# Kernel optimization log

Measured on AMD Instinct MI355X. Metric: run time of the kernel, lower is better.

## Reference

```python
import jax, jax.numpy as jnp
import numpy as np

KH = KW = 3  # kernel size for both convs


def conv2d_valid(x, w, b):
    # x: [B,C,H,W], w: [O,C,KH,KW], VALID padding, stride 1 (matches nn.Conv2d(3,18,3))
    y = jax.lax.conv_general_dilated(x, w, window_strides=(1, 1), padding='VALID',
                                     dimension_numbers=('NCHW', 'OIHW', 'NCHW'))
    return y + b[None, :, None, None]


def deform_conv2d(x, offset, w, b):
    # Faithful torchvision deform_conv2d: stride 1, pad 0, dilation 1, 1 group, 1 offset group.
    B, C, H, W = x.shape
    O = w.shape[0]
    Ho, Wo = offset.shape[2], offset.shape[3]
    K = KH * KW
    # offset layout: [B, 2*K, Ho, Wo], per-tap (dy, dx) interleaved, taps row-major
    off = offset.reshape(B, K, 2, Ho, Wo)
    dy, dx = off[:, :, 0], off[:, :, 1]                      # [B,K,Ho,Wo]
    ky = jnp.repeat(jnp.arange(KH), KW).astype(x.dtype)       # [K] tap row
    kx = jnp.tile(jnp.arange(KW), KH).astype(x.dtype)         # [K] tap col
    py = dy + jnp.arange(Ho, dtype=x.dtype)[None, None, :, None] + ky[None, :, None, None]
    px = dx + jnp.arange(Wo, dtype=x.dtype)[None, None, None, :] + kx[None, :, None, None]

    y0 = jnp.floor(py); x0 = jnp.floor(px)
    wy = py - y0; wx = px - x0                                # bilinear fractions
    y0i = y0.astype(jnp.int32); x0i = x0.astype(jnp.int32)

    x_flat = x.reshape(B, C, H * W)

    def corner(yi, xi):
        valid = ((yi >= 0) & (yi < H) & (xi >= 0) & (xi < W)).astype(x.dtype)  # zero pad outside
        idx = jnp.clip(yi, 0, H - 1) * W + jnp.clip(xi, 0, W - 1)              # [B,K,Ho,Wo]
        g = jax.vmap(lambda xf, ix: xf[:, ix])(x_flat, idx)                    # [B,C,K,Ho,Wo]
        return g * valid[:, None]

    val = (corner(y0i, x0i)         * ((1 - wy) * (1 - wx))[:, None]
         + corner(y0i, x0i + 1)     * ((1 - wy) * wx)[:, None]
         + corner(y0i + 1, x0i)     * (wy * (1 - wx))[:, None]
         + corner(y0i + 1, x0i + 1) * (wy * wx)[:, None])     # [B,C,K,Ho,Wo]

    out = jnp.einsum('bckhw,ock->bohw', val, w.reshape(O, C, K))
    return out + b[None, :, None, None]


def setup_inputs() -> dict:
    key = jax.random.key(0)
    k1, k2, k3, k4, k5 = jax.random.split(key, 5)
    B, C, H, W = 16, 3, 384, 384
    x = jax.random.normal(k1, (B, C, H, W), dtype=jnp.float32)
    # offset conv: Conv2d(3, 18, 3); scale down so learned offsets stay moderate
    conv_w = jax.random.normal(k2, (18, 3, KH, KW), dtype=jnp.float32) * 0.05
    conv_b = jax.random.normal(k3, (18,), dtype=jnp.float32) * 0.05
    # deform conv: DeformConv2d(3, 3, 3)
    dcn_w = jax.random.normal(k4, (3, 3, KH, KW), dtype=jnp.float32) * (1.0 / np.sqrt(3 * KH * KW))
    dcn_b = jax.random.normal(k5, (3,), dtype=jnp.float32) * 0.05
    return {'x': x, 'conv_w': conv_w, 'conv_b': conv_b, 'dcn_w': dcn_w, 'dcn_b': dcn_b}


def reference(x, conv_w, conv_b, dcn_w, dcn_b):
    offset = conv2d_valid(x, conv_w, conv_b)   # [B,18,H-2,W-2]
    return deform_conv2d(x, offset, dcn_w, dcn_b)  # [B,3,H-2,W-2]
```

## Files before the change

kernel.cpp:

```cpp
#include <hip/hip_runtime.h>

#define BATCH 16
#define CIN   3
#define H     384
#define W     384
#define HW    (H * W)
#define HO    382
#define WO    382
#define OFFC  18
#define OOUT  3
#define KTAPS 9

#define PAD   2
#define HP    (H + 2 * PAD)
#define WP    (W + 2 * PAD)

struct F3 { float a, b, c; };

__global__ __launch_bounds__(256)
void chw_to_hwc4_kernel(const float* __restrict__ x, float4* __restrict__ xt)
{
    const int gid = blockIdx.x * 256 + threadIdx.x;
    if (gid >= BATCH * HP * WP) return;
    const int b  = gid / (HP * WP);
    const int r2 = gid - b * (HP * WP);
    const int ry = r2 / WP;
    const int rx = r2 - ry * WP;
    const int yi = ry - PAD;
    const int xi = rx - PAD;
    float4 v = make_float4(0.f, 0.f, 0.f, 0.f);
    if ((unsigned)yi < (unsigned)H && (unsigned)xi < (unsigned)W) {
        const float* xb = x + (size_t)b * (CIN * HW);
        const int p = yi * W + xi;
        v.x = xb[p];
        v.y = xb[HW + p];
        v.z = xb[2 * HW + p];
    }
    xt[gid] = v;
}

__global__ __launch_bounds__(256)
void deform_pad4_kernel(const float4* __restrict__ xt,
                        const float* __restrict__ conv_w,
                        const float* __restrict__ conv_b,
                        const float* __restrict__ dcn_w,
                        const float* __restrict__ dcn_b,
                        float* __restrict__ out)
{
    const int total = BATCH * HO * WO;
    const int gid = blockIdx.x * 256 + threadIdx.x;
    if (gid >= total) return;

    const int wo  = gid % WO;
    const int tmp = gid / WO;
    const int ho  = tmp % HO;
    const int b   = tmp / HO;

    const float4* xtb = xt + (size_t)b * (HP * WP);

    float4 xp[3][3];
    #pragma unroll
    for (int i = 0; i < 3; ++i) {
        const float4* row = xtb + (ho + i + PAD) * WP + (wo + PAD);
        xp[i][0] = row[0];
        xp[i][1] = row[1];
        xp[i][2] = row[2];
    }

    float off[OFFC];
    #pragma unroll
    for (int o = 0; o < OFFC; ++o) {
        float a = conv_b[o];
        #pragma unroll
        for (int i = 0; i < 3; ++i)
            #pragma unroll
            for (int j = 0; j < 3; ++j) {
                a = fmaf(conv_w[o * 27 + 0 * 9 + i * 3 + j], xp[i][j].x, a);
                a = fmaf(conv_w[o * 27 + 1 * 9 + i * 3 + j], xp[i][j].y, a);
                a = fmaf(conv_w[o * 27 + 2 * 9 + i * 3 + j], xp[i][j].z, a);
            }
        off[o] = a;
    }

    float acc0 = dcn_b[0];
    float acc1 = dcn_b[1];
    float acc2 = dcn_b[2];

    #pragma unroll
    for (int k = 0; k < KTAPS; ++k) {
        const int ky = k / 3;
        const int kx = k % 3;
        const float oy = off[2 * k];
        const float ox = off[2 * k + 1];
        const float fy = floorf(oy);
        const float fx = floorf(ox);
        const float wy = oy - fy;
        const float wx = ox - fx;

        int iy = (int)fy + (ho + ky + PAD);
        int ix = (int)fx + (wo + kx + PAD);
        iy = min(max(iy, 0), HP - 2);
        ix = min(max(ix, 0), WP - 2);

        const float4* r0 = xtb + iy * WP + ix;
        const float4* r1 = r0 + WP;
        const float4 v00 = r0[0];
        const float4 v01 = r0[1];
        const float4 v10 = r1[0];
        const float4 v11 = r1[1];

        const float cwy = 1.f - wy;
        const float cwx = 1.f - wx;
        const float w00 = cwy * cwx;
        const float w01 = cwy * wx;
        const float w10 = wy * cwx;
        const float w11 = wy * wx;

        float s0 = v00.x * w00; s0 = fmaf(v01.x, w01, s0); s0 = fmaf(v10.x, w10, s0); s0 = fmaf(v11.x, w11, s0);
        float s1 = v00.y * w00; s1 = fmaf(v01.y, w01, s1); s1 = fmaf(v10.y, w10, s1); s1 = fmaf(v11.y, w11, s1);
        float s2 = v00.z * w00; s2 = fmaf(v01.z, w01, s2); s2 = fmaf(v10.z, w10, s2); s2 = fmaf(v11.z, w11, s2);

        acc0 = fmaf(dcn_w[0 * 27 + 0 * 9 + k], s0, acc0);
        acc0 = fmaf(dcn_w[0 * 27 + 1 * 9 + k], s1, acc0);
        acc0 = fmaf(dcn_w[0 * 27 + 2 * 9 + k], s2, acc0);
        acc1 = fmaf(dcn_w[1 * 27 + 0 * 9 + k], s0, acc1);
        acc1 = fmaf(dcn_w[1 * 27 + 1 * 9 + k], s1, acc1);
        acc1 = fmaf(dcn_w[1 * 27 + 2 * 9 + k], s2, acc1);
        acc2 = fmaf(dcn_w[2 * 27 + 0 * 9 + k], s0, acc2);
        acc2 = fmaf(dcn_w[2 * 27 + 1 * 9 + k], s1, acc2);
        acc2 = fmaf(dcn_w[2 * 27 + 2 * 9 + k], s2, acc2);
    }

    const int obase = b * (OOUT * HO * WO) + ho * WO + wo;
    __builtin_nontemporal_store(acc0, out + obase);
    __builtin_nontemporal_store(acc1, out + obase + HO * WO);
    __builtin_nontemporal_store(acc2, out + obase + 2 * HO * WO);
}

__global__ __launch_bounds__(256)
void chw_to_hwc_kernel(const float* __restrict__ x, float* __restrict__ xt)
{
    const int gid = blockIdx.x * 256 + threadIdx.x;
    if (gid >= BATCH * HW) return;
    const int b = gid / HW;
    const int p = gid - b * HW;
    const float* xb = x + (size_t)b * (CIN * HW);
    F3 v;
    v.a = xb[p];
    v.b = xb[HW + p];
    v.c = xb[2 * HW + p];
    *(F3*)(xt + (size_t)gid * 3) = v;
}

__global__ __launch_bounds__(256)
void deform_hwc_kernel(const float* __restrict__ xt,
                       const float* __restrict__ conv_w,
                       const float* __restrict__ conv_b,
                       const float* __restrict__ dcn_w,
                       const float* __restrict__ dcn_b,
                       float* __restrict__ out)
{
    const int total = BATCH * HO * WO;
    const int gid = blockIdx.x * 256 + threadIdx.x;
    if (gid >= total) return;

    const int wo  = gid % WO;
    const int tmp = gid / WO;
    const int ho  = tmp % HO;
    const int b   = tmp / HO;

    const float* xtb = xt + (size_t)b * (HW * 3);

    F3 xp[3][3];
    #pragma unroll
    for (int i = 0; i < 3; ++i)
        #pragma unroll
        for (int j = 0; j < 3; ++j)
            xp[i][j] = *(const F3*)(xtb + (size_t)((ho + i) * W + (wo + j)) * 3);

    float off[OFFC];
    #pragma unroll
    for (int o = 0; o < OFFC; ++o) {
        float a = conv_b[o];
        #pragma unroll
        for (int i = 0; i < 3; ++i)
            #pragma unroll
            for (int j = 0; j < 3; ++j) {
                a = fmaf(conv_w[o * 27 + 0 * 9 + i * 3 + j], xp[i][j].a, a);
                a = fmaf(conv_w[o * 27 + 1 * 9 + i * 3 + j], xp[i][j].b, a);
                a = fmaf(conv_w[o * 27 + 2 * 9 + i * 3 + j], xp[i][j].c, a);
            }
        off[o] = a;
    }

    float acc0 = dcn_b[0];
    float acc1 = dcn_b[1];
    float acc2 = dcn_b[2];

    #pragma unroll
    for (int k = 0; k < KTAPS; ++k) {
        const int ky = k / 3;
        const int kx = k % 3;
        const float py = off[2 * k]     + (float)(ho + ky);
        const float px = off[2 * k + 1] + (float)(wo + kx);
        const float y0f = floorf(py);
        const float x0f = floorf(px);
        const float wy = py - y0f;
        const float wx = px - x0f;
        const int y0 = (int)y0f;
        const int x0 = (int)x0f;
        const int y1 = y0 + 1;
        const int x1 = x0 + 1;
        const bool vy0 = (unsigned)y0 < (unsigned)H;
        const bool vy1 = (unsigned)y1 < (unsigned)H;
        const bool vx0 = (unsigned)x0 < (unsigned)W;
        const bool vx1 = (unsigned)x1 < (unsigned)W;
        const int cy0 = min(max(y0, 0), H - 1);
        const int cy1 = min(max(y1, 0), H - 1);
        const int cx0 = min(max(x0, 0), W - 1);
        const int cx1 = min(max(x1, 0), W - 1);
        const float w00 = (vy0 && vx0) ? (1.f - wy) * (1.f - wx) : 0.f;
        const float w01 = (vy0 && vx1) ? (1.f - wy) * wx         : 0.f;
        const float w10 = (vy1 && vx0) ? wy * (1.f - wx)         : 0.f;
        const float w11 = (vy1 && vx1) ? wy * wx                 : 0.f;

        const F3 v00 = *(const F3*)(xtb + (size_t)(cy0 * W + cx0) * 3);
        const F3 v01 = *(const F3*)(xtb + (size_t)(cy0 * W + cx1) * 3);
        const F3 v10 = *(const F3*)(xtb + (size_t)(cy1 * W + cx0) * 3);
        const F3 v11 = *(const F3*)(xtb + (size_t)(cy1 * W + cx1) * 3);

        float s0 = v00.a * w00; s0 = fmaf(v01.a, w01, s0); s0 = fmaf(v10.a, w10, s0); s0 = fmaf(v11.a, w11, s0);
        float s1 = v00.b * w00; s1 = fmaf(v01.b, w01, s1); s1 = fmaf(v10.b, w10, s1); s1 = fmaf(v11.b, w11, s1);
        float s2 = v00.c * w00; s2 = fmaf(v01.c, w01, s2); s2 = fmaf(v10.c, w10, s2); s2 = fmaf(v11.c, w11, s2);

        acc0 = fmaf(dcn_w[0 * 27 + 0 * 9 + k], s0, acc0);
        acc0 = fmaf(dcn_w[0 * 27 + 1 * 9 + k], s1, acc0);
        acc0 = fmaf(dcn_w[0 * 27 + 2 * 9 + k], s2, acc0);
        acc1 = fmaf(dcn_w[1 * 27 + 0 * 9 + k], s0, acc1);
        acc1 = fmaf(dcn_w[1 * 27 + 1 * 9 + k], s1, acc1);
        acc1 = fmaf(dcn_w[1 * 27 + 2 * 9 + k], s2, acc1);
        acc2 = fmaf(dcn_w[2 * 27 + 0 * 9 + k], s0, acc2);
        acc2 = fmaf(dcn_w[2 * 27 + 1 * 9 + k], s1, acc2);
        acc2 = fmaf(dcn_w[2 * 27 + 2 * 9 + k], s2, acc2);
    }

    const int obase = b * (OOUT * HO * WO) + ho * WO + wo;
    __builtin_nontemporal_store(acc0, out + obase);
    __builtin_nontemporal_store(acc1, out + obase + HO * WO);
    __builtin_nontemporal_store(acc2, out + obase + 2 * HO * WO);
}

__global__ __launch_bounds__(256)
void deform_fused_kernel(const float* __restrict__ x,
                         const float* __restrict__ conv_w,
                         const float* __restrict__ conv_b,
                         const float* __restrict__ dcn_w,
                         const float* __restrict__ dcn_b,
                         float* __restrict__ out)
{
    __shared__ float s_cw[OFFC * 27];
    __shared__ float s_cb[OFFC];
    __shared__ float s_dw[OOUT * 27];
    __shared__ float s_db[OOUT];

    const int t = threadIdx.x;
    for (int i = t; i < OFFC * 27; i += 256) s_cw[i] = conv_w[i];
    if (t < OFFC)      s_cb[t] = conv_b[t];
    if (t < OOUT * 27) s_dw[t] = dcn_w[t];
    if (t < OOUT)      s_db[t] = dcn_b[t];
    __syncthreads();

    const int total = BATCH * HO * WO;
    const int gid = blockIdx.x * 256 + t;
    if (gid >= total) return;

    const int wo  = gid % WO;
    const int tmp = gid / WO;
    const int ho  = tmp % HO;
    const int b   = tmp / HO;

    const float* xb = x + b * (CIN * HW);

    float xp[CIN][3][3];
    #pragma unroll
    for (int c = 0; c < CIN; ++c) {
        const float* xc = xb + c * HW + ho * W + wo;
        #pragma unroll
        for (int i = 0; i < 3; ++i)
            #pragma unroll
            for (int j = 0; j < 3; ++j)
                xp[c][i][j] = xc[i * W + j];
    }

    float off[OFFC];
    #pragma unroll
    for (int o = 0; o < OFFC; ++o) {
        float a = s_cb[o];
        const float* wv = &s_cw[o * 27];
        #pragma unroll
        for (int c = 0; c < CIN; ++c)
            #pragma unroll
            for (int i = 0; i < 3; ++i)
                #pragma unroll
                for (int j = 0; j < 3; ++j)
                    a = fmaf(wv[c * 9 + i * 3 + j], xp[c][i][j], a);
        off[o] = a;
    }

    float a0 = s_db[0], a1 = s_db[1], a2 = s_db[2];

    #pragma unroll
    for (int k = 0; k < KTAPS; ++k) {
        const int ky = k / 3;
        const int kx = k % 3;
        const float py = off[2 * k]     + (float)(ho + ky);
        const float px = off[2 * k + 1] + (float)(wo + kx);
        const float y0f = floorf(py);
        const float x0f = floorf(px);
        const float wy = py - y0f;
        const float wx = px - x0f;
        const int y0 = (int)y0f;
        const int x0 = (int)x0f;
        const int y1 = y0 + 1;
        const int x1 = x0 + 1;
        const bool vy0 = (unsigned)y0 < (unsigned)H;
        const bool vy1 = (unsigned)y1 < (unsigned)H;
        const bool vx0 = (unsigned)x0 < (unsigned)W;
        const bool vx1 = (unsigned)x1 < (unsigned)W;
        const int cy0 = min(max(y0, 0), H - 1);
        const int cy1 = min(max(y1, 0), H - 1);
        const int cx0 = min(max(x0, 0), W - 1);
        const int cx1 = min(max(x1, 0), W - 1);
        const float w00 = (vy0 && vx0) ? (1.f - wy) * (1.f - wx) : 0.f;
        const float w01 = (vy0 && vx1) ? (1.f - wy) * wx         : 0.f;
        const float w10 = (vy1 && vx0) ? wy * (1.f - wx)         : 0.f;
        const float w11 = (vy1 && vx1) ? wy * wx                 : 0.f;
        const int i00 = cy0 * W + cx0;
        const int i01 = cy0 * W + cx1;
        const int i10 = cy1 * W + cx0;
        const int i11 = cy1 * W + cx1;
        #pragma unroll
        for (int c = 0; c < CIN; ++c) {
            const float* xc = xb + c * HW;
            float s = xc[i00] * w00;
            s = fmaf(xc[i01], w01, s);
            s = fmaf(xc[i10], w10, s);
            s = fmaf(xc[i11], w11, s);
            a0 = fmaf(s_dw[0 * 27 + c * 9 + k], s, a0);
            a1 = fmaf(s_dw[1 * 27 + c * 9 + k], s, a1);
            a2 = fmaf(s_dw[2 * 27 + c * 9 + k], s, a2);
        }
    }

    const int obase = b * (OOUT * HO * WO) + ho * WO + wo;
    __builtin_nontemporal_store(a0, out + obase);
    __builtin_nontemporal_store(a1, out + obase + HO * WO);
    __builtin_nontemporal_store(a2, out + obase + 2 * HO * WO);
}

extern "C" void kernel_launch(void* const* d_in, const int* in_sizes, int n_in,
                              void* d_out, int out_size, void* d_ws, size_t ws_size,
                              hipStream_t stream) {
    const float* x      = (const float*)d_in[0];
    const float* conv_w = (const float*)d_in[1];
    const float* conv_b = (const float*)d_in[2];
    const float* dcn_w  = (const float*)d_in[3];
    const float* dcn_b  = (const float*)d_in[4];
    float* out = (float*)d_out;

    const int total = BATCH * HO * WO;
    const size_t need4 = (size_t)BATCH * HP * WP * sizeof(float4);
    const size_t need3 = (size_t)BATCH * HW * 3 * sizeof(float);

    if (ws_size >= need4) {
        float4* xt = (float4*)d_ws;
        const int cells = BATCH * HP * WP;
        chw_to_hwc4_kernel<<<(cells + 255) / 256, 256, 0, stream>>>(x, xt);
        deform_pad4_kernel<<<(total + 255) / 256, 256, 0, stream>>>(
            xt, conv_w, conv_b, dcn_w, dcn_b, out);
    } else if (ws_size >= need3) {
        float* xt = (float*)d_ws;
        chw_to_hwc_kernel<<<(BATCH * HW + 255) / 256, 256, 0, stream>>>(x, xt);
        deform_hwc_kernel<<<(total + 255) / 256, 256, 0, stream>>>(
            xt, conv_w, conv_b, dcn_w, dcn_b, out);
    } else {
        deform_fused_kernel<<<(total + 255) / 256, 256, 0, stream>>>(
            x, conv_w, conv_b, dcn_w, dcn_b, out);
    }
}
```

Before: 156.1 us.

## Compute two adjacent output pixels per thread using packed float2 math

Each thread now computes two horizontally adjacent output pixels. The offset conv, bilinear weights and output accumulation use two-wide float vectors so the compiler can emit packed FP32 FMA instructions. Neighbouring pixels share input loads (4 float4 per row instead of 6), and the output is written as float2 nontemporal stores. This halves the thread count and raises register pressure per thread, which may lower occupancy.

```diff
diff --git a/kernel.cpp b/kernel.cpp
--- a/kernel.cpp
+++ b/kernel.cpp
@@ -7,6 +7,7 @@
 #define HW    (H * W)
 #define HO    382
 #define WO    382
+#define WO2   191
 #define OFFC  18
 #define OOUT  3
 #define KTAPS 9
@@ -15,7 +16,10 @@
 #define HP    (H + 2 * PAD)
 #define WP    (W + 2 * PAD)
 
+typedef float vf2 __attribute__((ext_vector_type(2)));
 struct F3 { float a, b, c; };
+
+static __device__ __forceinline__ vf2 splat2(float s) { vf2 r; r.x = s; r.y = s; return r; }
 
 __global__ __launch_bounds__(256)
 void chw_to_hwc4_kernel(const float* __restrict__ x, float4* __restrict__ xt)
@@ -40,101 +44,146 @@
 }
 
 __global__ __launch_bounds__(256)
-void deform_pad4_kernel(const float4* __restrict__ xt,
+void deform_pair_kernel(const float4* __restrict__ xt,
                         const float* __restrict__ conv_w,
                         const float* __restrict__ conv_b,
                         const float* __restrict__ dcn_w,
                         const float* __restrict__ dcn_b,
                         float* __restrict__ out)
 {
-    const int total = BATCH * HO * WO;
+    const int total = BATCH * HO * WO2;
     const int gid = blockIdx.x * 256 + threadIdx.x;
     if (gid >= total) return;
 
-    const int wo  = gid % WO;
-    const int tmp = gid / WO;
+    const int g   = gid % WO2;
+    const int tmp = gid / WO2;
     const int ho  = tmp % HO;
     const int b   = tmp / HO;
+    const int wo  = 2 * g;
 
     const float4* xtb = xt + (size_t)b * (HP * WP);
 
-    float4 xp[3][3];
+    vf2 xp2[3][3][CIN];
     #pragma unroll
     for (int i = 0; i < 3; ++i) {
         const float4* row = xtb + (ho + i + PAD) * WP + (wo + PAD);
-        xp[i][0] = row[0];
-        xp[i][1] = row[1];
-        xp[i][2] = row[2];
-    }
-
-    float off[OFFC];
+        const float4 r0 = row[0];
+        const float4 r1 = row[1];
+        const float4 r2 = row[2];
+        const float4 r3 = row[3];
+        xp2[i][0][0].x = r0.x; xp2[i][0][0].y = r1.x;
+        xp2[i][0][1].x = r0.y; xp2[i][0][1].y = r1.y;
+        xp2[i][0][2].x = r0.z; xp2[i][0][2].y = r1.z;
+        xp2[i][1][0].x = r1.x; xp2[i][1][0].y = r2.x;
+        xp2[i][1][1].x = r1.y; xp2[i][1][1].y = r2.y;
+        xp2[i][1][2].x = r1.z; xp2[i][1][2].y = r2.z;
+        xp2[i][2][0].x = r2.x; xp2[i][2][0].y = r3.x;
+        xp2[i][2][1].x = r2.y; xp2[i][2][1].y = r3.y;
+        xp2[i][2][2].x = r2.z; xp2[i][2][2].y = r3.z;
+    }
+
+    vf2 off2[OFFC];
     #pragma unroll
     for (int o = 0; o < OFFC; ++o) {
-        float a = conv_b[o];
-        #pragma unroll
-        for (int i = 0; i < 3; ++i)
+        vf2 a = splat2(conv_b[o]);
+        #pragma unroll
+        for (int c = 0; c < CIN; ++c)
             #pragma unroll
-            for (int j = 0; j < 3; ++j) {
-                a = fmaf(conv_w[o * 27 + 0 * 9 + i * 3 + j], xp[i][j].x, a);
-                a = fmaf(conv_w[o * 27 + 1 * 9 + i * 3 + j], xp[i][j].y, a);
-                a = fmaf(conv_w[o * 27 + 2 * 9 + i * 3 + j], xp[i][j].z, a);
-            }
-        off[o] = a;
-    }
-
-    float acc0 = dcn_b[0];
-    float acc1 = dcn_b[1];
-    float acc2 = dcn_b[2];
+            for (int i = 0; i < 3; ++i)
+                #pragma unroll
+                for (int j = 0; j < 3; ++j)
+                    a = __builtin_elementwise_fma(splat2(conv_w[o * 27 + c * 9 + i * 3 + j]),
+                                                  xp2[i][j][c], a);
+        off2[o] = a;
+    }
+
+    vf2 acc0 = splat2(dcn_b[0]);
+    vf2 acc1 = splat2(dcn_b[1]);
+    vf2 acc2 = splat2(dcn_b[2]);
 
     #pragma unroll
     for (int k = 0; k < KTAPS; ++k) {
         const int ky = k / 3;
         const int kx = k % 3;
-        const float oy = off[2 * k];
-        const float ox = off[2 * k + 1];
-        const float fy = floorf(oy);
-        const float fx = floorf(ox);
-        const float wy = oy - fy;
-        const float wx = ox - fx;
-
-        int iy = (int)fy + (ho + ky + PAD);
-        int ix = (int)fx + (wo + kx + PAD);
-        iy = min(max(iy, 0), HP - 2);
-        ix = min(max(ix, 0), WP - 2);
-
-        const float4* r0 = xtb + iy * WP + ix;
-        const float4* r1 = r0 + WP;
-        const float4 v00 = r0[0];
-        const float4 v01 = r0[1];
-        const float4 v10 = r1[0];
-        const float4 v11 = r1[1];
-
-        const float cwy = 1.f - wy;
-        const float cwx = 1.f - wx;
-        const float w00 = cwy * cwx;
-        const float w01 = cwy * wx;
-        const float w10 = wy * cwx;
-        const float w11 = wy * wx;
-
-        float s0 = v00.x * w00; s0 = fmaf(v01.x, w01, s0); s0 = fmaf(v10.x, w10, s0); s0 = fmaf(v11.x, w11, s0);
-        float s1 = v00.y * w00; s1 = fmaf(v01.y, w01, s1); s1 = fmaf(v10.y, w10, s1); s1 = fmaf(v11.y, w11, s1);
-        float s2 = v00.z * w00; s2 = fmaf(v01.z, w01, s2); s2 = fmaf(v10.z, w10, s2); s2 = fmaf(v11.z, w11, s2);
-
-        acc0 = fmaf(dcn_w[0 * 27 + 0 * 9 + k], s0, acc0);
-        acc0 = fmaf(dcn_w[0 * 27 + 1 * 9 + k], s1, acc0);
-        acc0 = fmaf(dcn_w[0 * 27 + 2 * 9 + k], s2, acc0);
-        acc1 = fmaf(dcn_w[1 * 27 + 0 * 9 + k], s0, acc1);
-        acc1 = fmaf(dcn_w[1 * 27 + 1 * 9 + k], s1, acc1);
-        acc1 = fmaf(dcn_w[1 * 27 + 2 * 9 + k], s2, acc1);
-        acc2 = fmaf(dcn_w[2 * 27 + 0 * 9 + k], s0, acc2);
-        acc2 = fmaf(dcn_w[2 * 27 + 1 * 9 + k], s1, acc2);
-        acc2 = fmaf(dcn_w[2 * 27 + 2 * 9 + k], s2, acc2);
+        const vf2 oy = off2[2 * k];
+        const vf2 ox = off2[2 * k + 1];
+        const vf2 fy = __builtin_elementwise_floor(oy);
+        const vf2 fx = __builtin_elementwise_floor(ox);
+        const vf2 wy = oy - fy;
+        const vf2 wx = ox - fx;
+
+        const vf2 cwy = splat2(1.f) - wy;
+        const vf2 cwx = splat2(1.f) - wx;
+        const vf2 w00 = cwy * cwx;
+        const vf2 w01 = cwy * wx;
+        const vf2 w10 = wy * cwx;
+        const vf2 w11 = wy * wx;
+
+        int iy0 = (int)fy.x + (ho + ky + PAD);
+        int ix0 = (int)fx.x + (wo + kx + PAD);
+        int iy1 = (int)fy.y + (ho + ky + PAD);
+        int ix1 = (int)fx.y + (wo + 1 + kx + PAD);
+        iy0 = min(max(iy0, 0), HP - 2);
+        ix0 = min(max(ix0, 0), WP - 2);
+        iy1 = min(max(iy1, 0), HP - 2);
+        ix1 = min(max(ix1, 0), WP - 2);
+
+        const float4* p0r0 = xtb + iy0 * WP + ix0;
+        const float4* p0r1 = p0r0 + WP;
+        const float4* p1r0 = xtb + iy1 * WP + ix1;
+        const float4* p1r1 = p1r0 + WP;
+        const float4 a00 = p0r0[0];
+        const float4 a01 = p0r0[1];
+        const float4 a10 = p0r1[0];
+        const float4 a11 = p0r1[1];
+        const float4 b00 = p1r0[0];
+        const float4 b01 = p1r0[1];
+        const float4 b10 = p1r1[0];
+        const float4 b11 = p1r1[1];
+
+        vf2 v00, v01, v10, v11, s0, s1, s2;
+        v00.x = a00.x; v00.y = b00.x;
+        v01.x = a01.x; v01.y = b01.x;
+        v10.x = a10.x; v10.y = b10.x;
+        v11.x = a11.x; v11.y = b11.x;
+        s0 = v00 * w00;
+        s0 = __builtin_elementwise_fma(v01, w01, s0);
+        s0 = __builtin_elementwise_fma(v10, w10, s0);
+        s0 = __builtin_elementwise_fma(v11, w11, s0);
+
+        v00.x = a00.y; v00.y = b00.y;
+        v01.x = a01.y; v01.y = b01.y;
+        v10.x = a10.y; v10.y = b10.y;
+        v11.x = a11.y; v11.y = b11.y;
+        s1 = v00 * w00;
+        s1 = __builtin_elementwise_fma(v01, w01, s1);
+        s1 = __builtin_elementwise_fma(v10, w10, s1);
+        s1 = __builtin_elementwise_fma(v11, w11, s1);
+
+        v00.x = a00.z; v00.y = b00.z;
+        v01.x = a01.z; v01.y = b01.z;
+        v10.x = a10.z; v10.y = b10.z;
+        v11.x = a11.z; v11.y = b11.z;
+        s2 = v00 * w00;
+        s2 = __builtin_elementwise_fma(v01, w01, s2);
+        s2 = __builtin_elementwise_fma(v10, w10, s2);
+        s2 = __builtin_elementwise_fma(v11, w11, s2);
+
+        acc0 = __builtin_elementwise_fma(splat2(dcn_w[0 * 27 + 0 * 9 + k]), s0, acc0);
+        acc0 = __builtin_elementwise_fma(splat2(dcn_w[0 * 27 + 1 * 9 + k]), s1, acc0);
+        acc0 = __builtin_elementwise_fma(splat2(dcn_w[0 * 27 + 2 * 9 + k]), s2, acc0);
+        acc1 = __builtin_elementwise_fma(splat2(dcn_w[1 * 27 + 0 * 9 + k]), s0, acc1);
+        acc1 = __builtin_elementwise_fma(splat2(dcn_w[1 * 27 + 1 * 9 + k]), s1, acc1);
+        acc1 = __builtin_elementwise_fma(splat2(dcn_w[1 * 27 + 2 * 9 + k]), s2, acc1);
+        acc2 = __builtin_elementwise_fma(splat2(dcn_w[2 * 27 + 0 * 9 + k]), s0, acc2);
+        acc2 = __builtin_elementwise_fma(splat2(dcn_w[2 * 27 + 1 * 9 + k]), s1, acc2);
+        acc2 = __builtin_elementwise_fma(splat2(dcn_w[2 * 27 + 2 * 9 + k]), s2, acc2);
     }
 
     const int obase = b * (OOUT * HO * WO) + ho * WO + wo;
-    __builtin_nontemporal_store(acc0, out + obase);
-    __builtin_nontemporal_store(acc1, out + obase + HO * WO);
-    __builtin_nontemporal_store(acc2, out + obase + 2 * HO * WO);
+    __builtin_nontemporal_store(acc0, (vf2*)(out + obase));
+    __builtin_nontemporal_store(acc1, (vf2*)(out + obase + HO * WO));
+    __builtin_nontemporal_store(acc2, (vf2*)(out + obase + 2 * HO * WO));
 }
 
 __global__ __launch_bounds__(256)
@@ -376,7 +425,8 @@
         float4* xt = (float4*)d_ws;
         const int cells = BATCH * HP * WP;
         chw_to_hwc4_kernel<<<(cells + 255) / 256, 256, 0, stream>>>(x, xt);
-        deform_pad4_kernel<<<(total + 255) / 256, 256, 0, stream>>>(
+        const int pairs = BATCH * HO * WO2;
+        deform_pair_kernel<<<(pairs + 255) / 256, 256, 0, stream>>>(
             xt, conv_w, conv_b, dcn_w, dcn_b, out);
     } else if (ws_size >= need3) {
         float* xt = (float*)d_ws;
```

New measurement: 166.2 us. +6.5%, slower.
